# Performance work log

Measured on AMD Instinct MI355X. Metric: run time of the kernel, lower is better.

Reference implementation:

```python
import jax, jax.numpy as jnp
import numpy as np

B, C, H, W = 16, 512, 32, 32
NH = 8
HD = C // NH


def setup_inputs() -> dict:
    key = jax.random.key(0)
    k1, k2, k3 = jax.random.split(key, 3)
    x = jax.random.normal(k1, (B, C, H, W), dtype=jnp.float32)
    w_qkv = jax.random.normal(k2, (3 * C, C), dtype=jnp.float32) * (1.0 / np.sqrt(C))
    w_proj = jax.random.normal(k3, (C, C), dtype=jnp.float32) * (1.0 / np.sqrt(C))
    b_proj = jnp.zeros((C,), dtype=jnp.float32)
    return {"x": x, "w_qkv": w_qkv, "w_proj": w_proj, "b_proj": b_proj}


def reference(x, w_qkv, w_proj, b_proj):
    b, c, h, w = x.shape
    n = h * w
    # 1x1 conv qkv: (3C, C) applied per pixel
    qkv = jnp.einsum('oc,bchw->bohw', w_qkv, x)  # [B, 3C, H, W]
    qkv = qkv.reshape(b, 3, NH, HD, n)           # [B, 3, nh, hd, N]
    qkv = jnp.transpose(qkv, (1, 0, 2, 4, 3))    # [3, B, nh, N, hd]
    q, k, v = qkv[0], qkv[1], qkv[2]
    scale = HD ** -0.5
    scores = jnp.einsum('bhnd,bhmd->bhnm', q, k) * scale  # [B, nh, N, N]
    attn = jax.nn.softmax(scores, axis=-1)
    out = jnp.einsum('bhnm,bhmd->bhnd', attn, v)          # [B, nh, N, hd]
    out = jnp.transpose(out, (0, 1, 3, 2)).reshape(b, c, h, w)
    # 1x1 conv proj with bias
    out = jnp.einsum('oc,bchw->bohw', w_proj, out) + b_proj[None, :, None, None]
    return out
```

## Files before the change

### kernel.cpp

```cpp
#include <hip/hip_runtime.h>
#include <hip/hip_bf16.h>
#include <math.h>

#define BB 16
#define CC 512
#define NH 8
#define HD 64
#define NN 1024
#define THREEC 1536

#define QSCALE 0.18033688f

typedef __attribute__((ext_vector_type(8))) short bf16x8;
typedef __attribute__((ext_vector_type(4))) float f32x4;
typedef __attribute__((ext_vector_type(16))) float f32x16;

#if __has_builtin(__builtin_amdgcn_exp2f)
#define EXP2F __builtin_amdgcn_exp2f
#else
#define EXP2F exp2f
#endif

#define XT_OFF 0u
#define WQ_OFF 16777216u
#define WP_OFF 18350080u
#define QB_OFF 18874368u
#define KB_OFF 35651584u
#define VT_OFF 52428800u
#define AB_OFF 69206016u

static __device__ inline unsigned short f2bf(float f) {
  union { float f; unsigned u; } v; v.f = f;
  unsigned r = v.u + 0x7fffu + ((v.u >> 16) & 1u);
  return (unsigned short)(r >> 16);
}

static __device__ inline unsigned pk2bf(float a, float b) {
#if defined(__AMDGCN__) && __has_builtin(__builtin_amdgcn_cvt_pk_bf16_f32)
  typedef __attribute__((ext_vector_type(2))) __bf16 bfp2;
  union { bfp2 v; unsigned u; } z;
  z.v = __builtin_amdgcn_cvt_pk_bf16_f32(a, b);
  return z.u;
#else
  return (unsigned)f2bf(a) | ((unsigned)f2bf(b) << 16);
#endif
}

static __device__ inline void gld_lds16(const unsigned short* g, unsigned short* l) {
  __builtin_amdgcn_global_load_lds(
      (const __attribute__((address_space(1))) unsigned int*)g,
      (__attribute__((address_space(3))) unsigned int*)l, 16, 0, 0);
}

__global__ __launch_bounds__(256) void prep_fused(const float* __restrict__ x,
                                                  unsigned short* __restrict__ xT,
                                                  const float* __restrict__ wqkv,
                                                  const float* __restrict__ wproj,
                                                  unsigned short* __restrict__ dq,
                                                  unsigned short* __restrict__ dp) {
  const int b  = blockIdx.z;
  const int c0 = blockIdx.y * 64;
  const int n0 = blockIdx.x * 64;
  __shared__ float tile[64][65];
  const int t  = threadIdx.x;

  const int wid = (blockIdx.z * 8 + blockIdx.y) * 16 + blockIdx.x;
  if (wid < 512) {
    const size_t i8 = ((size_t)wid * 256 + t) * 8;
    const float* src;
    unsigned short* dst;
    if (i8 < 786432u) { src = wqkv + i8; dst = dq + i8; }
    else              { src = wproj + (i8 - 786432u); dst = dp + (i8 - 786432u); }
    float4 a = *(const float4*)src;
    float4 b4 = *(const float4*)(src + 4);
    unsigned short pk[8] = {f2bf(a.x), f2bf(a.y), f2bf(a.z), f2bf(a.w),
                            f2bf(b4.x), f2bf(b4.y), f2bf(b4.z), f2bf(b4.w)};
    *(uint4*)dst = *(const uint4*)pk;
  }

  const int cl = t >> 4, n4 = (t & 15) * 4;
#pragma unroll
  for (int r = 0; r < 4; ++r) {
    float4 v = *(const float4*)&x[((size_t)b * CC + c0 + cl + 16 * r) * NN + n0 + n4];
    *(float4*)&tile[cl + 16 * r][n4] = v;
  }
  __syncthreads();
  const int nl = t >> 4, c4 = (t & 15) * 4;
#pragma unroll
  for (int r = 0; r < 4; ++r) {
    ushort4 p;
    p.x = f2bf(tile[c4 + 0][nl + 16 * r]);
    p.y = f2bf(tile[c4 + 1][nl + 16 * r]);
    p.z = f2bf(tile[c4 + 2][nl + 16 * r]);
    p.w = f2bf(tile[c4 + 3][nl + 16 * r]);
    *(ushort4*)&xT[((size_t)b * NN + n0 + nl + 16 * r) * CC + c0 + c4] = p;
  }
}

__global__ __launch_bounds__(256) void qkv_mfma(const unsigned short* __restrict__ wq,
                                                const unsigned short* __restrict__ xT,
                                                unsigned short* __restrict__ qb,
                                                unsigned short* __restrict__ kb_,
                                                unsigned short* __restrict__ vt) {
  const int b  = blockIdx.z;
  const int o0 = blockIdx.y * 128;
  const int n0 = blockIdx.x * 128;
  const int t  = threadIdx.x;
  const int w    = t >> 6;
  const int lane = t & 63;
  const int quad = lane >> 4;
  const int l16  = lane & 15;
  const int m_off = (w >> 1) * 64;
  const int n_off = (w & 1) * 64;

  __shared__ unsigned short sm[17408];
  unsigned short* As = sm;
  unsigned short* Bs = sm + 8192;

  const int which = o0 >> 9;
  const bool vmode = (which == 2);

  const int srow = lane >> 3;
  const int ssw  = ((lane & 7) ^ srow) * 8;
  const unsigned short* gA = wq + (size_t)(o0 + 32 * w + srow) * CC + ssw;
  const unsigned short* gB = xT + ((size_t)b * NN + n0 + 32 * w + srow) * CC + ssw;

  f32x4 acc[4][4] = {};

  for (int c0 = 0; c0 < CC; c0 += 64) {
    __syncthreads();
#pragma unroll
    for (int L = 0; L < 4; ++L) {
      gld_lds16(gA + (size_t)(8 * L) * CC + c0, &As[(32 * w + 8 * L) * 64]);
      gld_lds16(gB + (size_t)(8 * L) * CC + c0, &Bs[(32 * w + 8 * L) * 64]);
    }
    __syncthreads();
    const unsigned short* Af = vmode ? Bs : As;
    const unsigned short* Bf = vmode ? As : Bs;
#pragma unroll
    for (int ks = 0; ks < 2; ++ks) {
      const int ph = ((ks * 4 + quad) ^ (l16 & 7)) * 8;
      bf16x8 af[4], bfr[4];
#pragma unroll
      for (int i = 0; i < 4; ++i) {
        af[i]  = *(const bf16x8*)&Af[(m_off + 16 * i + l16) * 64 + ph];
        bfr[i] = *(const bf16x8*)&Bf[(n_off + 16 * i + l16) * 64 + ph];
      }
#pragma unroll
      for (int i = 0; i < 4; ++i)
#pragma unroll
        for (int j = 0; j < 4; ++j)
          acc[i][j] = __builtin_amdgcn_mfma_f32_16x16x32_bf16(af[i], bfr[j], acc[i][j], 0, 0, 0);
    }
  }

  __syncthreads();
  const float sc = (which == 0) ? QSCALE : 1.0f;
#pragma unroll
  for (int i = 0; i < 4; ++i) {
#pragma unroll
    for (int j = 0; j < 4; ++j) {
      const int Drow = m_off + 16 * i + quad * 4;
      const int Dcol = n_off + 16 * j + l16;
      ushort4 p;
      p.x = f2bf(acc[i][j][0] * sc);
      p.y = f2bf(acc[i][j][1] * sc);
      p.z = f2bf(acc[i][j][2] * sc);
      p.w = f2bf(acc[i][j][3] * sc);
      *(ushort4*)&sm[Dcol * 136 + Drow] = p;
    }
  }
  __syncthreads();
  const int lrow = t >> 1;
  const int half = t & 1;
  const unsigned short* src = &sm[lrow * 136 + 64 * half];
  if (!vmode) {
    const int hh = ((o0 >> 6) & 7) + half;
    unsigned short* dst = (which == 0 ? qb : kb_) +
        ((size_t)(b * NH + hh) * NN + n0 + lrow) * HD;
#pragma unroll
    for (int i = 0; i < 8; ++i) *(uint4*)(dst + 8 * i) = *(const uint4*)(src + 8 * i);
  } else {
    const int hh = ((o0 + lrow) >> 6) & 7;
    const int d  = lrow & 63;
    unsigned short* dst = vt + ((size_t)(b * NH + hh) * HD + d) * NN + n0 + 64 * half;
#pragma unroll
    for (int i = 0; i < 8; ++i) *(uint4*)(dst + 8 * i) = *(const uint4*)(src + 8 * i);
  }
}

__global__ __launch_bounds__(256, 2) void attn_mfma(const unsigned short* __restrict__ Qg,
                                                    const unsigned short* __restrict__ Kg,
                                                    const unsigned short* __restrict__ Vtg,
                                                    unsigned short* __restrict__ attnB) {
  const int bh = blockIdx.x;
  const int b  = bh >> 3;
  const int h  = bh & 7;
  const int n0 = blockIdx.y * 256;
  const int t  = threadIdx.x;
  const int w    = t >> 6;
  const int lane = t & 63;
  const int l31  = lane & 31;
  const int hi   = lane >> 5;

  __shared__ unsigned short sm[32768];

  const unsigned short* qrow = Qg + ((size_t)bh * NN + n0 + w * 64 + l31) * HD + hi * 8;
  bf16x8 qfA[4], qfB[4];
#pragma unroll
  for (int c = 0; c < 4; ++c) {
    qfA[c] = *(const bf16x8*)(qrow + 16 * c);
    qfB[c] = *(const bf16x8*)(qrow + 32 * HD + 16 * c);
  }

  const int krow = (l31 & ~12) | ((l31 & 4) << 1) | ((l31 & 8) >> 1);
  const int ksw  = (krow >> 2) & 7;
  const int vsw  = (l31 >> 2) & 7;

  const f32x16 fz = {};
  f32x16 oaccA[2] = {}, oaccB[2] = {};
  float lxA = 0.f, lyA = 0.f, lxB = 0.f, lyB = 0.f;

  const int srow = lane >> 3;
  const int sgA  = (lane & 7) ^ ((4 * w + (srow >> 2)) & 7);
  const int sgB  = (lane & 7) ^ ((4 * w + 2 + (srow >> 2)) & 7);
  const unsigned short* kstA = Kg + (size_t)bh * NN * HD +
                               (size_t)(16 * w + srow) * HD + sgA * 8;
  const unsigned short* kstB = Kg + (size_t)bh * NN * HD +
                               (size_t)(16 * w + 8 + srow) * HD + sgB * 8;
  const unsigned short* vstA = Vtg + (size_t)bh * HD * NN +
                               (size_t)(16 * w + srow) * NN + sgA * 8;
  const unsigned short* vstB = Vtg + (size_t)bh * HD * NN +
                               (size_t)(16 * w + 8 + srow) * NN + sgB * 8;
  const int kso0 = (16 * w) * 64;
  const int kso1 = (16 * w + 8) * 64;

  auto stage = [&](int j0, int p) {
#pragma unroll
    for (int hf = 0; hf < 2; ++hf) {
      unsigned short* Kp = sm + p * 8192 + hf * 4096;
      unsigned short* Vp = sm + 16384 + p * 8192 + hf * 4096;
      const int jo = j0 + 64 * hf;
      gld_lds16(kstA + (size_t)jo * HD, Kp + kso0);
      gld_lds16(kstB + (size_t)jo * HD, Kp + kso1);
      gld_lds16(vstA + jo, Vp + kso0);
      gld_lds16(vstB + jo, Vp + kso1);
    }
  };

  stage(0, 0);
  int cur = 0;

#pragma unroll 1
  for (int j0 = 0; j0 < NN; j0 += 128) {
    __syncthreads();
    if (j0 + 128 < NN) stage(j0 + 128, cur ^ 1);

#pragma unroll
    for (int hf = 0; hf < 2; ++hf) {
      const unsigned short* Ks = sm + cur * 8192 + hf * 4096;
      const unsigned short* Vt = sm + 16384 + cur * 8192 + hf * 4096;

#pragma unroll
      for (int kb = 0; kb < 2; ++kb) {
        const unsigned short* krp = &Ks[(32 * kb + krow) * 64];
        __builtin_amdgcn_s_setprio(1);
        bf16x8 kf0 = *(const bf16x8*)(krp + (((0 + hi) ^ ksw) * 8));
        f32x16 stA = __builtin_amdgcn_mfma_f32_32x32x16_bf16(kf0, qfA[0], fz, 0, 0, 0);
        f32x16 stB = __builtin_amdgcn_mfma_f32_32x32x16_bf16(kf0, qfB[0], fz, 0, 0, 0);
#pragma unroll
        for (int c = 1; c < 4; ++c) {
          bf16x8 kf = *(const bf16x8*)(krp + (((2 * c + hi) ^ ksw) * 8));
          stA = __builtin_amdgcn_mfma_f32_32x32x16_bf16(kf, qfA[c], stA, 0, 0, 0);
          stB = __builtin_amdgcn_mfma_f32_32x32x16_bf16(kf, qfB[c], stB, 0, 0, 0);
        }
        __builtin_amdgcn_s_setprio(0);
        unsigned PA[8], PB[8];
#pragma unroll
        for (int i = 0; i < 8; ++i) {
          float ea = EXP2F(stA[2 * i]);
          float eb = EXP2F(stA[2 * i + 1]);
          lxA += ea; lyA += eb;
          PA[i] = pk2bf(ea, eb);
        }
#pragma unroll
        for (int i = 0; i < 8; ++i) {
          float ea = EXP2F(stB[2 * i]);
          float eb = EXP2F(stB[2 * i + 1]);
          lxB += ea; lyB += eb;
          PB[i] = pk2bf(ea, eb);
        }

        __builtin_amdgcn_s_setprio(1);
#pragma unroll
        for (int g = 0; g < 2; ++g) {
          union { unsigned u[4]; bf16x8 v; } cvA, cvB;
          cvA.u[0] = PA[4 * g + 0]; cvA.u[1] = PA[4 * g + 1];
          cvA.u[2] = PA[4 * g + 2]; cvA.u[3] = PA[4 * g + 3];
          cvB.u[0] = PB[4 * g + 0]; cvB.u[1] = PB[4 * g + 1];
          cvB.u[2] = PB[4 * g + 2]; cvB.u[3] = PB[4 * g + 3];
#pragma unroll
          for (int mt = 0; mt < 2; ++mt) {
            const int vrow = 32 * mt + l31;
            bf16x8 vf = *(const bf16x8*)&Vt[vrow * 64 + (((4 * kb + 2 * g + hi) ^ vsw) * 8)];
            oaccA[mt] = __builtin_amdgcn_mfma_f32_32x32x16_bf16(vf, cvA.v, oaccA[mt], 0, 0, 0);
            oaccB[mt] = __builtin_amdgcn_mfma_f32_32x32x16_bf16(vf, cvB.v, oaccB[mt], 0, 0, 0);
          }
        }
        __builtin_amdgcn_s_setprio(0);
      }
    }
    cur ^= 1;
  }

  float lsA = lxA + lyA;
  lsA += __shfl_xor(lsA, 32);
  const float invA = 1.0f / lsA;
  float lsB = lxB + lyB;
  lsB += __shfl_xor(lsB, 32);
  const float invB = 1.0f / lsB;

  __syncthreads();
  unsigned short* Es = sm + w * 2304;
  const int q    = lane >> 1;
  const int half = lane & 1;
  const unsigned short* esrc = &Es[q * 72 + 32 * half];

#pragma unroll
  for (int mt = 0; mt < 2; ++mt) {
#pragma unroll
    for (int rr = 0; rr < 4; ++rr) {
      const int d = 32 * mt + 8 * rr + 4 * hi;
      ushort4 p;
      p.x = f2bf(oaccA[mt][4 * rr + 0] * invA);
      p.y = f2bf(oaccA[mt][4 * rr + 1] * invA);
      p.z = f2bf(oaccA[mt][4 * rr + 2] * invA);
      p.w = f2bf(oaccA[mt][4 * rr + 3] * invA);
      *(ushort4*)&Es[l31 * 72 + d] = p;
    }
  }
  {
    unsigned short* gdst = attnB + ((size_t)b * NN + n0 + w * 64 + q) * CC + h * HD + 32 * half;
#pragma unroll
    for (int i = 0; i < 4; ++i) *(uint4*)(gdst + 8 * i) = *(const uint4*)(esrc + 8 * i);
  }

#pragma unroll
  for (int mt = 0; mt < 2; ++mt) {
#pragma unroll
    for (int rr = 0; rr < 4; ++rr) {
      const int d = 32 * mt + 8 * rr + 4 * hi;
      ushort4 p;
      p.x = f2bf(oaccB[mt][4 * rr + 0] * invB);
      p.y = f2bf(oaccB[mt][4 * rr + 1] * invB);
      p.z = f2bf(oaccB[mt][4 * rr + 2] * invB);
      p.w = f2bf(oaccB[mt][4 * rr + 3] * invB);
      *(ushort4*)&Es[l31 * 72 + d] = p;
    }
  }
  {
    unsigned short* gdst = attnB + ((size_t)b * NN + n0 + w * 64 + 32 + q) * CC + h * HD + 32 * half;
#pragma unroll
    for (int i = 0; i < 4; ++i) *(uint4*)(gdst + 8 * i) = *(const uint4*)(esrc + 8 * i);
  }
}

__global__ __launch_bounds__(256) void proj_mfma(const unsigned short* __restrict__ wp,
                                                 const unsigned short* __restrict__ aB,
                                                 const float* __restrict__ bias,
                                                 float* __restrict__ out) {
  const int b  = blockIdx.z;
  const int o0 = blockIdx.y * 128;
  const int n0 = blockIdx.x * 128;
  const int t  = threadIdx.x;
  const int w    = t >> 6;
  const int lane = t & 63;
  const int quad = lane >> 4;
  const int l16  = lane & 15;
  const int m_off = (w >> 1) * 64;
  const int n_off = (w & 1) * 64;

  __shared__ unsigned short sm[16384];
  unsigned short* As = sm;
  unsigned short* Bs = sm + 8192;

  const int srow = lane >> 3;
  const int ssw  = ((lane & 7) ^ srow) * 8;
  const unsigned short* gA = wp + (size_t)(o0 + 32 * w + srow) * CC + ssw;
  const unsigned short* gB = aB + ((size_t)b * NN + n0 + 32 * w + srow) * CC + ssw;

  f32x4 acc[4][4] = {};

  for (int c0 = 0; c0 < CC; c0 += 64) {
    __syncthreads();
#pragma unroll
    for (int L = 0; L < 4; ++L) {
      gld_lds16(gA + (size_t)(8 * L) * CC + c0, &As[(32 * w + 8 * L) * 64]);
      gld_lds16(gB + (size_t)(8 * L) * CC + c0, &Bs[(32 * w + 8 * L) * 64]);
    }
    __syncthreads();
#pragma unroll
    for (int ks = 0; ks < 2; ++ks) {
      const int ph = ((ks * 4 + quad) ^ (l16 & 7)) * 8;
      bf16x8 af[4], bfr[4];
#pragma unroll
      for (int i = 0; i < 4; ++i) {
        af[i]  = *(const bf16x8*)&As[(m_off + 16 * i + l16) * 64 + ph];
        bfr[i] = *(const bf16x8*)&Bs[(n_off + 16 * i + l16) * 64 + ph];
      }
#pragma unroll
      for (int i = 0; i < 4; ++i)
#pragma unroll
        for (int j = 0; j < 4; ++j)
          acc[i][j] = __builtin_amdgcn_mfma_f32_16x16x32_bf16(af[i], bfr[j], acc[i][j], 0, 0, 0);
    }
  }

#pragma unroll
  for (int i = 0; i < 4; ++i) {
#pragma unroll
    for (int r = 0; r < 4; ++r) {
      const int o = o0 + m_off + 16 * i + quad * 4 + r;
      const float bv = bias[o];
      float* orow = out + ((size_t)b * CC + o) * NN + n0 + n_off;
#pragma unroll
      for (int j = 0; j < 4; ++j)
        orow[16 * j + l16] = acc[i][j][r] + bv;
    }
  }
}

extern "C" void kernel_launch(void* const* d_in, const int* in_sizes, int n_in,
                              void* d_out, int out_size, void* d_ws, size_t ws_size,
                              hipStream_t stream) {
  const float* x      = (const float*)d_in[0];
  const float* w_qkv  = (const float*)d_in[1];
  const float* w_proj = (const float*)d_in[2];
  const float* b_proj = (const float*)d_in[3];
  char* wsb  = (char*)d_ws;
  float* out = (float*)d_out;

  unsigned short* xT  = (unsigned short*)(wsb + XT_OFF);
  unsigned short* wq  = (unsigned short*)(wsb + WQ_OFF);
  unsigned short* wp  = (unsigned short*)(wsb + WP_OFF);
  unsigned short* qb  = (unsigned short*)(wsb + QB_OFF);
  unsigned short* kb_ = (unsigned short*)(wsb + KB_OFF);
  unsigned short* vt  = (unsigned short*)(wsb + VT_OFF);
  unsigned short* aB  = (unsigned short*)(wsb + AB_OFF);

  prep_fused<<<dim3(16, 8, BB), 256, 0, stream>>>(x, xT, w_qkv, w_proj, wq, wp);
  qkv_mfma<<<dim3(8, 12, BB), 256, 0, stream>>>(wq, xT, qb, kb_, vt);
  attn_mfma<<<dim3(BB * NH, NN / 256), 256, 0, stream>>>(qb, kb_, vt, aB);
  proj_mfma<<<dim3(8, 4, BB), 256, 0, stream>>>(wp, aB, b_proj, out);
}
```

Measured before the change: 188.7 us.

## Split attention KV range across two wave groups with LDS reduction

The attention kernel now runs 512 threads per block. Two groups of four waves each process half of the key/value sequence for the same query rows, and their partial output accumulators and row sums are combined through shared memory before normalization and store. This doubles the waves available to hide MFMA and exp latency on the 512-block grid, which otherwise underfills the GPU. The cost is an extra reduction phase with several barriers and LDS traffic, plus a tighter register budget under the new launch bounds.

Result: slower. 496.5 us (+163.1%).

```diff
diff --git a/kernel.cpp b/kernel.cpp
--- a/kernel.cpp
+++ b/kernel.cpp
@@ -189,7 +189,7 @@
   }
 }
 
-__global__ __launch_bounds__(256, 2) void attn_mfma(const unsigned short* __restrict__ Qg,
+__global__ __launch_bounds__(512, 4) void attn_mfma(const unsigned short* __restrict__ Qg,
                                                     const unsigned short* __restrict__ Kg,
                                                     const unsigned short* __restrict__ Vtg,
                                                     unsigned short* __restrict__ attnB) {
@@ -199,13 +199,15 @@
   const int n0 = blockIdx.y * 256;
   const int t  = threadIdx.x;
   const int w    = t >> 6;
+  const int s    = w >> 2;
+  const int ws   = w & 3;
   const int lane = t & 63;
   const int l31  = lane & 31;
   const int hi   = lane >> 5;
 
   __shared__ unsigned short sm[32768];
 
-  const unsigned short* qrow = Qg + ((size_t)bh * NN + n0 + w * 64 + l31) * HD + hi * 8;
+  const unsigned short* qrow = Qg + ((size_t)bh * NN + n0 + ws * 64 + l31) * HD + hi * 8;
   bf16x8 qfA[4], qfB[4];
 #pragma unroll
   for (int c = 0; c < 4; ++c) {
@@ -222,146 +224,195 @@
   float lxA = 0.f, lyA = 0.f, lxB = 0.f, lyB = 0.f;
 
   const int srow = lane >> 3;
-  const int sgA  = (lane & 7) ^ ((4 * w + (srow >> 2)) & 7);
-  const int sgB  = (lane & 7) ^ ((4 * w + 2 + (srow >> 2)) & 7);
+  const int sgA  = (lane & 7) ^ ((4 * ws + (srow >> 2)) & 7);
+  const int sgB  = (lane & 7) ^ ((4 * ws + 2 + (srow >> 2)) & 7);
+  const int kbase = s * 512;
   const unsigned short* kstA = Kg + (size_t)bh * NN * HD +
-                               (size_t)(16 * w + srow) * HD + sgA * 8;
+                               (size_t)(kbase + 16 * ws + srow) * HD + sgA * 8;
   const unsigned short* kstB = Kg + (size_t)bh * NN * HD +
-                               (size_t)(16 * w + 8 + srow) * HD + sgB * 8;
+                               (size_t)(kbase + 16 * ws + 8 + srow) * HD + sgB * 8;
   const unsigned short* vstA = Vtg + (size_t)bh * HD * NN +
-                               (size_t)(16 * w + srow) * NN + sgA * 8;
+                               (size_t)(16 * ws + srow) * NN + kbase + sgA * 8;
   const unsigned short* vstB = Vtg + (size_t)bh * HD * NN +
-                               (size_t)(16 * w + 8 + srow) * NN + sgB * 8;
-  const int kso0 = (16 * w) * 64;
-  const int kso1 = (16 * w + 8) * 64;
+                               (size_t)(16 * ws + 8 + srow) * NN + kbase + sgB * 8;
+  const int kso0 = (16 * ws) * 64;
+  const int kso1 = (16 * ws + 8) * 64;
 
   auto stage = [&](int j0, int p) {
-#pragma unroll
-    for (int hf = 0; hf < 2; ++hf) {
-      unsigned short* Kp = sm + p * 8192 + hf * 4096;
-      unsigned short* Vp = sm + 16384 + p * 8192 + hf * 4096;
-      const int jo = j0 + 64 * hf;
-      gld_lds16(kstA + (size_t)jo * HD, Kp + kso0);
-      gld_lds16(kstB + (size_t)jo * HD, Kp + kso1);
-      gld_lds16(vstA + jo, Vp + kso0);
-      gld_lds16(vstB + jo, Vp + kso1);
-    }
+    unsigned short* Kp = sm + (2 * s + p) * 4096;
+    unsigned short* Vp = sm + 16384 + (2 * s + p) * 4096;
+    gld_lds16(kstA + (size_t)j0 * HD, Kp + kso0);
+    gld_lds16(kstB + (size_t)j0 * HD, Kp + kso1);
+    gld_lds16(vstA + j0, Vp + kso0);
+    gld_lds16(vstB + j0, Vp + kso1);
   };
 
   stage(0, 0);
   int cur = 0;
 
 #pragma unroll 1
-  for (int j0 = 0; j0 < NN; j0 += 128) {
+  for (int j0 = 0; j0 < 512; j0 += 64) {
     __syncthreads();
-    if (j0 + 128 < NN) stage(j0 + 128, cur ^ 1);
-
-#pragma unroll
-    for (int hf = 0; hf < 2; ++hf) {
-      const unsigned short* Ks = sm + cur * 8192 + hf * 4096;
-      const unsigned short* Vt = sm + 16384 + cur * 8192 + hf * 4096;
-
-#pragma unroll
-      for (int kb = 0; kb < 2; ++kb) {
-        const unsigned short* krp = &Ks[(32 * kb + krow) * 64];
-        __builtin_amdgcn_s_setprio(1);
-        bf16x8 kf0 = *(const bf16x8*)(krp + (((0 + hi) ^ ksw) * 8));
-        f32x16 stA = __builtin_amdgcn_mfma_f32_32x32x16_bf16(kf0, qfA[0], fz, 0, 0, 0);
-        f32x16 stB = __builtin_amdgcn_mfma_f32_32x32x16_bf16(kf0, qfB[0], fz, 0, 0, 0);
-#pragma unroll
-        for (int c = 1; c < 4; ++c) {
-          bf16x8 kf = *(const bf16x8*)(krp + (((2 * c + hi) ^ ksw) * 8));
-          stA = __builtin_amdgcn_mfma_f32_32x32x16_bf16(kf, qfA[c], stA, 0, 0, 0);
-          stB = __builtin_amdgcn_mfma_f32_32x32x16_bf16(kf, qfB[c], stB, 0, 0, 0);
+    if (j0 + 64 < 512) stage(j0 + 64, cur ^ 1);
+
+    const unsigned short* Ks = sm + (2 * s + cur) * 4096;
+    const unsigned short* Vt = sm + 16384 + (2 * s + cur) * 4096;
+
+#pragma unroll
+    for (int kb = 0; kb < 2; ++kb) {
+      const unsigned short* krp = &Ks[(32 * kb + krow) * 64];
+      __builtin_amdgcn_s_setprio(1);
+      bf16x8 kf0 = *(const bf16x8*)(krp + (((0 + hi) ^ ksw) * 8));
+      f32x16 stA = __builtin_amdgcn_mfma_f32_32x32x16_bf16(kf0, qfA[0], fz, 0, 0, 0);
+      f32x16 stB = __builtin_amdgcn_mfma_f32_32x32x16_bf16(kf0, qfB[0], fz, 0, 0, 0);
+#pragma unroll
+      for (int c = 1; c < 4; ++c) {
+        bf16x8 kf = *(const bf16x8*)(krp + (((2 * c + hi) ^ ksw) * 8));
+        stA = __builtin_amdgcn_mfma_f32_32x32x16_bf16(kf, qfA[c], stA, 0, 0, 0);
+        stB = __builtin_amdgcn_mfma_f32_32x32x16_bf16(kf, qfB[c], stB, 0, 0, 0);
+      }
+      __builtin_amdgcn_s_setprio(0);
+      unsigned PA[8], PB[8];
+#pragma unroll
+      for (int i = 0; i < 8; ++i) {
+        float ea = EXP2F(stA[2 * i]);
+        float eb = EXP2F(stA[2 * i + 1]);
+        lxA += ea; lyA += eb;
+        PA[i] = pk2bf(ea, eb);
+      }
+#pragma unroll
+      for (int i = 0; i < 8; ++i) {
+        float ea = EXP2F(stB[2 * i]);
+        float eb = EXP2F(stB[2 * i + 1]);
+        lxB += ea; lyB += eb;
+        PB[i] = pk2bf(ea, eb);
+      }
+
+      __builtin_amdgcn_s_setprio(1);
+#pragma unroll
+      for (int g = 0; g < 2; ++g) {
+        union { unsigned u[4]; bf16x8 v; } cvA, cvB;
+        cvA.u[0] = PA[4 * g + 0]; cvA.u[1] = PA[4 * g + 1];
+        cvA.u[2] = PA[4 * g + 2]; cvA.u[3] = PA[4 * g + 3];
+        cvB.u[0] = PB[4 * g + 0]; cvB.u[1] = PB[4 * g + 1];
+        cvB.u[2] = PB[4 * g + 2]; cvB.u[3] = PB[4 * g + 3];
+#pragma unroll
+        for (int mt = 0; mt < 2; ++mt) {
+          const int vrow = 32 * mt + l31;
+          bf16x8 vf = *(const bf16x8*)&Vt[vrow * 64 + (((4 * kb + 2 * g + hi) ^ vsw) * 8)];
+          oaccA[mt] = __builtin_amdgcn_mfma_f32_32x32x16_bf16(vf, cvA.v, oaccA[mt], 0, 0, 0);
+          oaccB[mt] = __builtin_amdgcn_mfma_f32_32x32x16_bf16(vf, cvB.v, oaccB[mt], 0, 0, 0);
         }
-        __builtin_amdgcn_s_setprio(0);
-        unsigned PA[8], PB[8];
-#pragma unroll
-        for (int i = 0; i < 8; ++i) {
-          float ea = EXP2F(stA[2 * i]);
-          float eb = EXP2F(stA[2 * i + 1]);
-          lxA += ea; lyA += eb;
-          PA[i] = pk2bf(ea, eb);
-        }
-#pragma unroll
-        for (int i = 0; i < 8; ++i) {
-          float ea = EXP2F(stB[2 * i]);
-          float eb = EXP2F(stB[2 * i + 1]);
-          lxB += ea; lyB += eb;
-          PB[i] = pk2bf(ea, eb);
-        }
-
-        __builtin_amdgcn_s_setprio(1);
-#pragma unroll
-        for (int g = 0; g < 2; ++g) {
-          union { unsigned u[4]; bf16x8 v; } cvA, cvB;
-          cvA.u[0] = PA[4 * g + 0]; cvA.u[1] = PA[4 * g + 1];
-          cvA.u[2] = PA[4 * g + 2]; cvA.u[3] = PA[4 * g + 3];
-          cvB.u[0] = PB[4 * g + 0]; cvB.u[1] = PB[4 * g + 1];
-          cvB.u[2] = PB[4 * g + 2]; cvB.u[3] = PB[4 * g + 3];
-#pragma unroll
-          for (int mt = 0; mt < 2; ++mt) {
-            const int vrow = 32 * mt + l31;
-            bf16x8 vf = *(const bf16x8*)&Vt[vrow * 64 + (((4 * kb + 2 * g + hi) ^ vsw) * 8)];
-            oaccA[mt] = __builtin_amdgcn_mfma_f32_32x32x16_bf16(vf, cvA.v, oaccA[mt], 0, 0, 0);
-            oaccB[mt] = __builtin_amdgcn_mfma_f32_32x32x16_bf16(vf, cvB.v, oaccB[mt], 0, 0, 0);
-          }
-        }
-        __builtin_amdgcn_s_setprio(0);
-      }
+      }
+      __builtin_amdgcn_s_setprio(0);
     }
     cur ^= 1;
   }
 
-  float lsA = lxA + lyA;
-  lsA += __shfl_xor(lsA, 32);
-  const float invA = 1.0f / lsA;
-  float lsB = lxB + lyB;
-  lsB += __shfl_xor(lsB, 32);
-  const float invB = 1.0f / lsB;
-
-  __syncthreads();
-  unsigned short* Es = sm + w * 2304;
-  const int q    = lane >> 1;
-  const int half = lane & 1;
-  const unsigned short* esrc = &Es[q * 72 + 32 * half];
-
-#pragma unroll
-  for (int mt = 0; mt < 2; ++mt) {
-#pragma unroll
-    for (int rr = 0; rr < 4; ++rr) {
-      const int d = 32 * mt + 8 * rr + 4 * hi;
-      ushort4 p;
-      p.x = f2bf(oaccA[mt][4 * rr + 0] * invA);
-      p.y = f2bf(oaccA[mt][4 * rr + 1] * invA);
-      p.z = f2bf(oaccA[mt][4 * rr + 2] * invA);
-      p.w = f2bf(oaccA[mt][4 * rr + 3] * invA);
-      *(ushort4*)&Es[l31 * 72 + d] = p;
-    }
-  }
-  {
-    unsigned short* gdst = attnB + ((size_t)b * NN + n0 + w * 64 + q) * CC + h * HD + 32 * half;
-#pragma unroll
-    for (int i = 0; i < 4; ++i) *(uint4*)(gdst + 8 * i) = *(const uint4*)(esrc + 8 * i);
-  }
-
-#pragma unroll
-  for (int mt = 0; mt < 2; ++mt) {
-#pragma unroll
-    for (int rr = 0; rr < 4; ++rr) {
-      const int d = 32 * mt + 8 * rr + 4 * hi;
-      ushort4 p;
-      p.x = f2bf(oaccB[mt][4 * rr + 0] * invB);
-      p.y = f2bf(oaccB[mt][4 * rr + 1] * invB);
-      p.z = f2bf(oaccB[mt][4 * rr + 2] * invB);
-      p.w = f2bf(oaccB[mt][4 * rr + 3] * invB);
-      *(ushort4*)&Es[l31 * 72 + d] = p;
-    }
-  }
-  {
-    unsigned short* gdst = attnB + ((size_t)b * NN + n0 + w * 64 + 32 + q) * CC + h * HD + 32 * half;
-#pragma unroll
-    for (int i = 0; i < 4; ++i) *(uint4*)(gdst + 8 * i) = *(const uint4*)(esrc + 8 * i);
+  float plA = lxA + lyA;
+  float plB = lxB + lyB;
+  float* CB = (float*)sm;
+
+  __syncthreads();
+  if (s == 1) {
+    float* R = CB + ws * 2176;
+#pragma unroll
+    for (int mt = 0; mt < 2; ++mt)
+#pragma unroll
+      for (int r = 0; r < 8; ++r)
+        *(float2*)&R[lane * 34 + mt * 16 + 2 * r] =
+            make_float2(oaccA[mt][2 * r], oaccA[mt][2 * r + 1]);
+    CB[8704 + ws * 128 + lane * 2 + 0] = plA;
+    CB[8704 + ws * 128 + lane * 2 + 1] = plB;
+  }
+  __syncthreads();
+  if (s == 0) {
+    float* R = CB + ws * 2176;
+#pragma unroll
+    for (int mt = 0; mt < 2; ++mt)
+#pragma unroll
+      for (int r = 0; r < 8; ++r) {
+        float2 v = *(const float2*)&R[lane * 34 + mt * 16 + 2 * r];
+        oaccA[mt][2 * r]     += v.x;
+        oaccA[mt][2 * r + 1] += v.y;
+      }
+    plA += CB[8704 + ws * 128 + lane * 2 + 0];
+    plB += CB[8704 + ws * 128 + lane * 2 + 1];
+  }
+  __syncthreads();
+  if (s == 1) {
+    float* R = CB + ws * 2176;
+#pragma unroll
+    for (int mt = 0; mt < 2; ++mt)
+#pragma unroll
+      for (int r = 0; r < 8; ++r)
+        *(float2*)&R[lane * 34 + mt * 16 + 2 * r] =
+            make_float2(oaccB[mt][2 * r], oaccB[mt][2 * r + 1]);
+  }
+  __syncthreads();
+  if (s == 0) {
+    float* R = CB + ws * 2176;
+#pragma unroll
+    for (int mt = 0; mt < 2; ++mt)
+#pragma unroll
+      for (int r = 0; r < 8; ++r) {
+        float2 v = *(const float2*)&R[lane * 34 + mt * 16 + 2 * r];
+        oaccB[mt][2 * r]     += v.x;
+        oaccB[mt][2 * r + 1] += v.y;
+      }
+  }
+  __syncthreads();
+
+  if (s == 0) {
+    float lsA = plA;
+    lsA += __shfl_xor(lsA, 32);
+    const float invA = 1.0f / lsA;
+    float lsB = plB;
+    lsB += __shfl_xor(lsB, 32);
+    const float invB = 1.0f / lsB;
+
+    unsigned short* Es = sm + ws * 2304;
+    const int q    = lane >> 1;
+    const int half = lane & 1;
+    const unsigned short* esrc = &Es[q * 72 + 32 * half];
+
+#pragma unroll
+    for (int mt = 0; mt < 2; ++mt) {
+#pragma unroll
+      for (int rr = 0; rr < 4; ++rr) {
+        const int d = 32 * mt + 8 * rr + 4 * hi;
+        ushort4 p;
+        p.x = f2bf(oaccA[mt][4 * rr + 0] * invA);
+        p.y = f2bf(oaccA[mt][4 * rr + 1] * invA);
+        p.z = f2bf(oaccA[mt][4 * rr + 2] * invA);
+        p.w = f2bf(oaccA[mt][4 * rr + 3] * invA);
+        *(ushort4*)&Es[l31 * 72 + d] = p;
+      }
+    }
+    {
+      unsigned short* gdst = attnB + ((size_t)b * NN + n0 + ws * 64 + q) * CC + h * HD + 32 * half;
+#pragma unroll
+      for (int i = 0; i < 4; ++i) *(uint4*)(gdst + 8 * i) = *(const uint4*)(esrc + 8 * i);
+    }
+
+#pragma unroll
+    for (int mt = 0; mt < 2; ++mt) {
+#pragma unroll
+      for (int rr = 0; rr < 4; ++rr) {
+        const int d = 32 * mt + 8 * rr + 4 * hi;
+        ushort4 p;
+        p.x = f2bf(oaccB[mt][4 * rr + 0] * invB);
+        p.y = f2bf(oaccB[mt][4 * rr + 1] * invB);
+        p.z = f2bf(oaccB[mt][4 * rr + 2] * invB);
+        p.w = f2bf(oaccB[mt][4 * rr + 3] * invB);
+        *(ushort4*)&Es[l31 * 72 + d] = p;
+      }
+    }
+    {
+      unsigned short* gdst = attnB + ((size_t)b * NN + n0 + ws * 64 + 32 + q) * CC + h * HD + 32 * half;
+#pragma unroll
+      for (int i = 0; i < 4; ++i) *(uint4*)(gdst + 8 * i) = *(const uint4*)(esrc + 8 * i);
+    }
   }
 }
 
@@ -450,6 +501,6 @@
 
   prep_fused<<<dim3(16, 8, BB), 256, 0, stream>>>(x, xT, w_qkv, w_proj, wq, wp);
   qkv_mfma<<<dim3(8, 12, BB), 256, 0, stream>>>(wq, xT, qb, kb_, vt);
-  attn_mfma<<<dim3(BB * NH, NN / 256), 256, 0, stream>>>(qb, kb_, vt, aB);
+  attn_mfma<<<dim3(BB * NH, NN / 256), 512, 0, stream>>>(qb, kb_, vt, aB);
   proj_mfma<<<dim3(8, 4, BB), 256, 0, stream>>>(wp, aB, b_proj, out);
 }
```
